# Performance work log

Measured on AMD Instinct MI355X. Metric: run time of the kernel, lower is better.

The kernel has to match this reference:

```python
import jax, jax.numpy as jnp
import numpy as np


def setup_inputs() -> dict:
    key = jax.random.key(0)
    ks = jax.random.split(key, 8)
    B, C, H, W = 4, 256, 56, 56
    Cq = C // 8
    s = 0.05  # small init scale for conv weights, like kaiming-ish for 1x1 convs
    return {
        "x": jax.random.normal(ks[0], (B, C, H, W), jnp.float32),
        "Wq": jax.random.normal(ks[1], (Cq, C), jnp.float32) * s,
        "bq": jax.random.normal(ks[2], (Cq,), jnp.float32) * s,
        "Wk": jax.random.normal(ks[3], (Cq, C), jnp.float32) * s,
        "bk": jax.random.normal(ks[4], (Cq,), jnp.float32) * s,
        "Wv": jax.random.normal(ks[5], (C, C), jnp.float32) * s,
        "bv": jax.random.normal(ks[6], (C,), jnp.float32) * s,
        "gamma": jax.random.normal(ks[7], (1,), jnp.float32),
    }


def reference(x, Wq, bq, Wk, bk, Wv, bv, gamma):
    B, C, H, W = x.shape
    N = H * W
    xf = x.reshape(B, C, N)  # flatten spatial

    # 1x1 convs == channel matmuls
    q = jnp.einsum('oc,bcn->bon', Wq, xf) + bq[None, :, None]   # [B,Cq,N]
    k = jnp.einsum('oc,bcn->bon', Wk, xf) + bk[None, :, None]   # [B,Cq,N]
    v = jnp.einsum('oc,bcn->bon', Wv, xf) + bv[None, :, None]   # [B,C,N]

    # lipschitz_norm from weights: u=||Q||_F, v=max row-norm of K^T, w=max row-norm of V^T
    u = jnp.linalg.norm(Wq)
    vn = jnp.max(jnp.linalg.norm(Wk.T, axis=1))
    wn = jnp.max(jnp.linalg.norm(Wv.T, axis=1))
    norm_value = jnp.maximum(u * vn, u * wn)  # maximum(u*v, v*u, u*w)

    # energy[b,i,j] = <q[:,i], k[:,j]>, scaled by custom Lipschitz norm
    energy = jnp.einsum('bci,bcj->bij', q, k) / norm_value      # [B,N,N]
    attention = jax.nn.softmax(energy, axis=-1)

    # out[b,c,i] = sum_j v[b,c,j] * attention[b,i,j]
    out = jnp.einsum('bcj,bij->bci', v, attention).reshape(B, C, H, W)

    # lipschitz_bound: exp(sqrt(3)) * sqrt(N/C) + 2*sqrt(6)
    bound = np.float32(np.exp(np.sqrt(3.0)) * np.sqrt(N / C) + 2.0 * np.sqrt(6.0))
    out = out / bound

    return gamma * out + x
```

## Files before the change

### kernel.cpp

```cpp
#include <hip/hip_runtime.h>

#define N_SP 3136
#define C_CH 256
#define CQ   32
#define NB   4
#define JT   64
#define NJT  49
#define QT   64
#define INV_BOUND 0.04051569f
#define LOG2E 1.44269504f

typedef __attribute__((ext_vector_type(8))) short bf16x8;
typedef __attribute__((ext_vector_type(4))) float f32x4;
typedef __attribute__((ext_vector_type(2))) long long l64x2;
typedef unsigned short u16;
typedef unsigned int   u32;
typedef unsigned char  u8;
typedef long long      l64;

#define MFMA16(a,b,c) __builtin_amdgcn_mfma_f32_16x16x32_bf16(a,b,c,0,0,0)
#define MFMA8(a,b,c)  __builtin_amdgcn_mfma_f32_16x16x32_bf8_fp8(a,b,c,0,0,0)

__device__ __forceinline__ u16 f2b(float f) {
    u32 u = __builtin_bit_cast(u32, f);
    u += 0x7fffu + ((u >> 16) & 1u);
    return (u16)(u >> 16);
}
__device__ __forceinline__ u8 f2fp8(float f) {
    return (u8)(__builtin_amdgcn_cvt_pk_fp8_f32(f, f, 0, false) & 0xff);
}
__device__ __forceinline__ void dma16(const void* g, void* l) {
    __builtin_amdgcn_global_load_lds((const __attribute__((address_space(1))) u32*)g,
                                     (__attribute__((address_space(3))) u32*)l, 16, 0, 0);
}
__device__ __forceinline__ void dma4(const void* g, void* l) {
    __builtin_amdgcn_global_load_lds((const __attribute__((address_space(1))) u32*)g,
                                     (__attribute__((address_space(3))) u32*)l, 4, 0, 0);
}

__global__ __launch_bounds__(256) void stage1_kernel(
    const float* __restrict__ x, const float* __restrict__ Wq,
    const float* __restrict__ Wk, const float* __restrict__ Wv,
    u8* __restrict__ xT, u8* __restrict__ Wqb, u8* __restrict__ Wkb,
    u8* __restrict__ Wvb, float* __restrict__ scale_out,
    float* __restrict__ kmax)
{
    __shared__ float smem[64 * 65];
    const int t = threadIdx.x;
    const int bid = blockIdx.x;

    if (bid < 784) {
        float (*tile)[65] = (float(*)[65])smem;
        const int xcd = bid & 7, slot = bid >> 3;
        const int b = xcd >> 1;
        const int i = slot * 2 + (xcd & 1);
        const int ct = i & 3, nt = i >> 2;
        const int c0 = ct * 64, n0 = nt * 64;
        const int cc = t >> 4, nn4 = (t & 15) * 4;
        #pragma unroll
        for (int k = 0; k < 4; ++k) {
            int cl = cc + k * 16;
            float4 v = *(const float4*)(x + (size_t)(b * C_CH + c0 + cl) * N_SP + n0 + nn4);
            tile[cl][nn4] = v.x; tile[cl][nn4 + 1] = v.y;
            tile[cl][nn4 + 2] = v.z; tile[cl][nn4 + 3] = v.w;
        }
        __syncthreads();
        const int c4 = (t & 15) * 4, nn = t >> 4;
        #pragma unroll
        for (int k = 0; k < 4; ++k) {
            int nl = nn + k * 16;
            ushort4 o;
            o.x = f2b(tile[c4 + 0][nl]); o.y = f2b(tile[c4 + 1][nl]);
            o.z = f2b(tile[c4 + 2][nl]); o.w = f2b(tile[c4 + 3][nl]);
            const int off = ((c0 + c4) * 2) ^ ((nl & 15) << 5);
            *(ushort4*)(xT + (size_t)(b * N_SP + n0 + nl) * 512 + off) = o;
        }
    } else if (bid < 864) {
        int idx = (bid - 784) * 256 + t;
        const float* src; u8* dst; int off;
        if (idx < 2048)      { src = Wq; dst = Wqb; off = idx; }
        else if (idx < 4096) { src = Wk; dst = Wkb; off = idx - 2048; }
        else                 { src = Wv; dst = Wvb; off = idx - 4096; }
        float4 v = *(const float4*)(src + off * 4);
        ushort4 o; o.x = f2b(v.x); o.y = f2b(v.y); o.z = f2b(v.z); o.w = f2b(v.w);
        const int row = off >> 6, inner = (off & 63) * 8;
        *(ushort4*)(dst + row * 512 + (inner ^ ((row & 15) << 5))) = o;
    } else {
        if (t < NB) kmax[t] = 0.f;
        float* red = smem;
        float u2 = 0.f;
        for (int i = t; i < CQ * C_CH; i += 256) { float w = Wq[i]; u2 += w * w; }
        red[t] = u2; __syncthreads();
        #pragma unroll
        for (int s = 128; s > 0; s >>= 1) { if (t < s) red[t] += red[t + s]; __syncthreads(); }
        float u2t = red[0]; __syncthreads();
        float vn2 = 0.f;
        for (int o = 0; o < CQ; ++o)   { float w = Wk[o * C_CH + t]; vn2 += w * w; }
        float wn2 = 0.f;
        for (int o = 0; o < C_CH; ++o) { float w = Wv[o * C_CH + t]; wn2 += w * w; }
        red[t] = fmaxf(vn2, wn2); __syncthreads();
        #pragma unroll
        for (int s = 128; s > 0; s >>= 1) { if (t < s) red[t] = fmaxf(red[t], red[t + s]); __syncthreads(); }
        if (t == 0) scale_out[0] = 1.0f / (sqrtf(u2t) * sqrtf(red[0]));
    }
}

__global__ __launch_bounds__(256) void qkv_mfma(
    const u8* __restrict__ xT, const u8* __restrict__ Wqb,
    const u8* __restrict__ Wkb, const u8* __restrict__ Wvb,
    const float* __restrict__ bq, const float* __restrict__ bk,
    const float* __restrict__ bv, const float* __restrict__ scale_p,
    u16* __restrict__ qT, u8* __restrict__ Kg, u8* __restrict__ Vg,
    float* __restrict__ qnorm, float* __restrict__ kmax)
{
    __shared__ __align__(16) u8 xTl[32768];
    __shared__ __align__(16) u8 Wl[32768];

    const int t = threadIdx.x;
    const int xcd = blockIdx.x & 7, slot = blockIdx.x >> 3;
    const int b = xcd >> 1;
    const int i = slot * 2 + (xcd & 1);
    if (i >= 245) return;
    const int split = i / 49, nt = i % 49;
    const int w = t >> 6, lane = t & 63, li = t & 15, g = (t >> 4) & 3;
    const int n = nt * 64 + w * 16 + li;
    const int r0 = (split - 1) * 64;
    const f32x4 zero = {0.f, 0.f, 0.f, 0.f};

    {
        const u8* xsrc = xT + (size_t)(b * N_SP + nt * 64) * 512;
        #pragma unroll
        for (int k = 0; k < 8; ++k)
            dma16(xsrc + w * 8192 + k * 1024 + lane * 16, xTl + w * 8192 + k * 1024);
        if (split == 0) {
            #pragma unroll
            for (int k = 0; k < 4; ++k)
                dma16(Wqb + w * 4096 + k * 1024 + lane * 16, Wl + w * 4096 + k * 1024);
            #pragma unroll
            for (int k = 0; k < 4; ++k)
                dma16(Wkb + w * 4096 + k * 1024 + lane * 16, Wl + 16384 + w * 4096 + k * 1024);
        } else {
            const u8* wsrc = Wvb + (size_t)r0 * 512;
            #pragma unroll
            for (int k = 0; k < 8; ++k)
                dma16(wsrc + w * 8192 + k * 1024 + lane * 16, Wl + w * 8192 + k * 1024);
        }
    }
    asm volatile("s_waitcnt vmcnt(0)" ::: "memory");
    __syncthreads();

    const int swz = li << 5;
    bf16x8 xf[8];
    #pragma unroll
    for (int ks = 0; ks < 8; ++ks)
        xf[ks] = *(const bf16x8*)(xTl + (w * 16 + li) * 512 + ((ks * 64 + 16 * g) ^ swz));

    if (split == 0) {
        f32x4 aq0 = zero, aq1 = zero, ak0 = zero, ak1 = zero;
        #pragma unroll
        for (int ks = 0; ks < 8; ++ks) {
            const int o = (ks * 64 + 16 * g) ^ swz;
            bf16x8 w0 = *(const bf16x8*)(Wl + li * 512 + o);
            bf16x8 w1 = *(const bf16x8*)(Wl + (16 + li) * 512 + o);
            bf16x8 w2 = *(const bf16x8*)(Wl + 16384 + li * 512 + o);
            bf16x8 w3 = *(const bf16x8*)(Wl + 16384 + (16 + li) * 512 + o);
            aq0 = MFMA16(w0, xf[ks], aq0);
            aq1 = MFMA16(w1, xf[ks], aq1);
            ak0 = MFMA16(w2, xf[ks], ak0);
            ak1 = MFMA16(w3, xf[ks], ak1);
        }
        const float scf = scale_p[0] * LOG2E;
        f32x4 bq0 = *(const f32x4*)(bq + 4 * g);
        f32x4 bq1 = *(const f32x4*)(bq + 16 + 4 * g);
        f32x4 bk0 = *(const f32x4*)(bk + 4 * g);
        f32x4 bk1 = *(const f32x4*)(bk + 16 + 4 * g);
        float qn2 = 0.f, kn2 = 0.f;
        ushort4 s0, s1;
        #pragma unroll
        for (int r = 0; r < 4; ++r) {
            float q0 = (aq0[r] + bq0[r]) * scf;
            float q1 = (aq1[r] + bq1[r]) * scf;
            qn2 += q0 * q0 + q1 * q1;
            ((u16*)&s0)[r] = f2b(q0); ((u16*)&s1)[r] = f2b(q1);
        }
        *(ushort4*)(qT + (size_t)(b * N_SP + n) * CQ + 4 * g)      = s0;
        *(ushort4*)(qT + (size_t)(b * N_SP + n) * CQ + 16 + 4 * g) = s1;
        #pragma unroll
        for (int r = 0; r < 4; ++r) {
            float k0 = ak0[r] + bk0[r];
            float k1 = ak1[r] + bk1[r];
            kn2 += k0 * k0 + k1 * k1;
            ((u16*)&s0)[r] = f2b(k0); ((u16*)&s1)[r] = f2b(k1);
        }
        u8* krow = Kg + ((size_t)b * N_SP + n) * 64;
        const int swn = ((n >> 1) & 3) << 4;
        *(ushort4*)(krow + ((8 * g) ^ swn))      = s0;
        *(ushort4*)(krow + ((32 + 8 * g) ^ swn)) = s1;

        qn2 += __shfl_xor(qn2, 16); qn2 += __shfl_xor(qn2, 32);
        kn2 += __shfl_xor(kn2, 16); kn2 += __shfl_xor(kn2, 32);
        if (g == 0) qnorm[b * N_SP + n] = sqrtf(qn2);
        float kn = sqrtf(kn2);
        #pragma unroll
        for (int d = 1; d < 16; d <<= 1) kn = fmaxf(kn, __shfl_xor(kn, d));
        if ((t & 63) == 0) atomicMax((int*)(kmax + b), __float_as_int(kn));
    } else {
        f32x4 a[4] = {zero, zero, zero, zero};
        #pragma unroll
        for (int ks = 0; ks < 8; ++ks) {
            const int o = (ks * 64 + 16 * g) ^ swz;
            #pragma unroll
            for (int fr = 0; fr < 4; ++fr) {
                bf16x8 wf = *(const bf16x8*)(Wl + (fr * 16 + li) * 512 + o);
                a[fr] = MFMA16(wf, xf[ks], a[fr]);
            }
        }
        const int jj = w * 16 + li;
        const int p = ((jj >> 5) & 1) * 8 + ((jj >> 3) & 3) * 16 + (jj & 7);
        u8* vtile = Vg + (size_t)(b * NJT + nt) * 16384;
        #pragma unroll
        for (int fr = 0; fr < 4; ++fr) {
            f32x4 bb = *(const f32x4*)(bv + r0 + fr * 16 + 4 * g);
            #pragma unroll
            for (int r = 0; r < 4; ++r) {
                const int c = r0 + fr * 16 + 4 * g + r;
                vtile[c * 64 + (p ^ (((c >> 1) & 3) << 4))] = f2fp8(a[fr][r] + bb[r]);
            }
        }
    }
}

__global__ __launch_bounds__(512) void attn_mfma(
    const u16* __restrict__ qT, const u8* __restrict__ Kg,
    const u8* __restrict__ Vg, const float* __restrict__ x,
    const float* __restrict__ gamma_p, const float* __restrict__ qnorm,
    const float* __restrict__ kmax, float* __restrict__ out)
{
    __shared__ __align__(16) u8 smem[86016];
    u8* const Vl = smem;
    u8* const Kl = smem + 65536;
    u8* const Pl = smem + 81920;

    const int t = threadIdx.x;
    const int w = t >> 6, li = t & 15, g = (t >> 4) & 3;
    const int jh = w & 3, qh = w >> 2;
    const int cw = w * 32;
    const int swz = ((li >> 1) & 3) << 4;

    const int xcd = blockIdx.x & 7, slot = blockIdx.x >> 3;
    const int b  = xcd >> 1;
    const int qt = slot * 2 + (xcd & 1);
    if (qt >= NJT) return;
    const int i0 = qt * QT;

    const u16* qTb = qT + (size_t)b * N_SP * CQ;
    const u8*  Kbb = Kg + (size_t)b * N_SP * 64;
    const u8*  Vbb = Vg + (size_t)b * NJT * 16384;
    const float kmb = kmax[b];
    const f32x4 zero = {0.f, 0.f, 0.f, 0.f};

    const int qA = 2 * qh, qB = 2 * qh + 1;
    const bf16x8 qfA = *(const bf16x8*)(qTb + (size_t)(i0 + qA * 16 + li) * CQ + 8 * g);
    const bf16x8 qfB = *(const bf16x8*)(qTb + (size_t)(i0 + qB * 16 + li) * CQ + 8 * g);
    const float mrA = qnorm[b * N_SP + i0 + qA * 16 + li] * kmb;
    const float mrB = qnorm[b * N_SP + i0 + qB * 16 + li] * kmb;

    f32x4 acc[4][2];
    #pragma unroll
    for (int qq = 0; qq < 4; ++qq) { acc[qq][0] = zero; acc[qq][1] = zero; }
    float lsA = 0.f, lsB = 0.f;

    #define ISSUE(jt_, s_) do {                                               \
        const u8* vsrc_ = Vbb + (size_t)(jt_) * 16384;                        \
        const u8* ksrc_ = Kbb + (size_t)(jt_) * 4096;                         \
        _Pragma("unroll")                                                     \
        for (int i_ = 0; i_ < 2; ++i_)                                        \
            dma16(vsrc_ + i_ * 8192 + t * 16,                                 \
                  Vl + (s_) * 16384 + i_ * 8192 + w * 1024);                  \
        _Pragma("unroll")                                                     \
        for (int i_ = 0; i_ < 2; ++i_)                                        \
            dma4(ksrc_ + i_ * 2048 + t * 4,                                   \
                 Kl + (s_) * 4096 + i_ * 2048 + w * 256);                     \
    } while (0)

    ISSUE(0, 0);
    ISSUE(1, 1);
    ISSUE(2, 2);

    const int p0 = ((jh >> 1) & 1) * 8 + ((jh * 2 + (g >> 1)) & 3) * 16 + 4 * (g & 1);

    for (int it = 0; it < NJT; ++it) {
        const int cur = it & 3;
        asm volatile("s_waitcnt vmcnt(8) lgkmcnt(0)" ::: "memory");
        __builtin_amdgcn_s_barrier();
        asm volatile("" ::: "memory");

        {
            int jn = it + 3; if (jn > NJT - 1) jn = NJT - 1;
            ISSUE(jn, (cur + 3) & 3);
        }

        const u8* Kc = Kl + cur * 4096;
        bf16x8 kf = *(const bf16x8*)(Kc + (jh * 16 + li) * 64 + ((16 * g) ^ swz));
        f32x4 sA = MFMA16(kf, qfA, zero);
        f32x4 sB = MFMA16(kf, qfB, zero);
        {
            float a0 = exp2f(sA[0] - mrA), a1 = exp2f(sA[1] - mrA);
            float a2 = exp2f(sA[2] - mrA), a3 = exp2f(sA[3] - mrA);
            lsA += (a0 + a1) + (a2 + a3);
            int pk = __builtin_amdgcn_cvt_pk_bf8_f32(a0, a1, 0, false);
            pk = __builtin_amdgcn_cvt_pk_bf8_f32(a2, a3, pk, true);
            *(u32*)(Pl + (qA * 16 + li) * 64 + (p0 ^ swz)) = (u32)pk;
            float b0 = exp2f(sB[0] - mrB), b1 = exp2f(sB[1] - mrB);
            float b2 = exp2f(sB[2] - mrB), b3 = exp2f(sB[3] - mrB);
            lsB += (b0 + b1) + (b2 + b3);
            pk = __builtin_amdgcn_cvt_pk_bf8_f32(b0, b1, 0, false);
            pk = __builtin_amdgcn_cvt_pk_bf8_f32(b2, b3, pk, true);
            *(u32*)(Pl + (qB * 16 + li) * 64 + (p0 ^ swz)) = (u32)pk;
        }
        asm volatile("s_waitcnt lgkmcnt(0)" ::: "memory");
        __builtin_amdgcn_s_barrier();
        asm volatile("" ::: "memory");

        const u8* Vc = Vl + cur * 16384;
        __builtin_amdgcn_s_setprio(1);
        l64x2 pa0 = *(const l64x2*)(Pl + (0 * 16 + li) * 64 + ((16 * g) ^ swz));
        l64x2 pa1 = *(const l64x2*)(Pl + (1 * 16 + li) * 64 + ((16 * g) ^ swz));
        l64x2 pa2 = *(const l64x2*)(Pl + (2 * 16 + li) * 64 + ((16 * g) ^ swz));
        l64x2 pa3 = *(const l64x2*)(Pl + (3 * 16 + li) * 64 + ((16 * g) ^ swz));
        l64x2 v0  = *(const l64x2*)(Vc + (cw + li) * 64 + ((16 * g) ^ swz));
        l64x2 v1  = *(const l64x2*)(Vc + (cw + 16 + li) * 64 + ((16 * g) ^ swz));
        acc[0][0] = MFMA8(pa0[0], v0[0], acc[0][0]);
        acc[0][1] = MFMA8(pa0[0], v1[0], acc[0][1]);
        acc[1][0] = MFMA8(pa1[0], v0[0], acc[1][0]);
        acc[1][1] = MFMA8(pa1[0], v1[0], acc[1][1]);
        acc[2][0] = MFMA8(pa2[0], v0[0], acc[2][0]);
        acc[2][1] = MFMA8(pa2[0], v1[0], acc[2][1]);
        acc[3][0] = MFMA8(pa3[0], v0[0], acc[3][0]);
        acc[3][1] = MFMA8(pa3[0], v1[0], acc[3][1]);
        acc[0][0] = MFMA8(pa0[1], v0[1], acc[0][0]);
        acc[0][1] = MFMA8(pa0[1], v1[1], acc[0][1]);
        acc[1][0] = MFMA8(pa1[1], v0[1], acc[1][0]);
        acc[1][1] = MFMA8(pa1[1], v1[1], acc[1][1]);
        acc[2][0] = MFMA8(pa2[1], v0[1], acc[2][0]);
        acc[2][1] = MFMA8(pa2[1], v1[1], acc[2][1]);
        acc[3][0] = MFMA8(pa3[1], v0[1], acc[3][0]);
        acc[3][1] = MFMA8(pa3[1], v1[1], acc[3][1]);
        __builtin_amdgcn_s_setprio(0);
    }
    #undef ISSUE

    lsA += __shfl_xor(lsA, 16); lsA += __shfl_xor(lsA, 32);
    lsB += __shfl_xor(lsB, 16); lsB += __shfl_xor(lsB, 32);
    __syncthreads();
    float* red       = (float*)Pl;
    float* red_final = (float*)(Pl + 1024);
    if ((t & 63) < 16) {
        red[w * 32 + li]      = lsA;
        red[w * 32 + 16 + li] = lsB;
    }
    __syncthreads();
    if (t < 64) {
        const int h = t >> 4, l2 = t & 15;
        float s = 0.f;
        #pragma unroll
        for (int jw = 0; jw < 4; ++jw)
            s += red[((h >> 1) * 4 + jw) * 32 + (h & 1) * 16 + l2];
        red_final[t] = s;
    }
    __syncthreads();

    const float gsc = gamma_p[0] * INV_BOUND;
    #pragma unroll
    for (int qq = 0; qq < 4; ++qq) {
        f32x4 lsv = *(const f32x4*)(red_final + qq * 16 + 4 * g);
        f32x4 rinv;
        #pragma unroll
        for (int r = 0; r < 4; ++r) rinv[r] = gsc / lsv[r];
        #pragma unroll
        for (int cf = 0; cf < 2; ++cf) {
            const int c = cw + cf * 16 + li;
            const size_t base = ((size_t)b * C_CH + c) * N_SP + i0 + qq * 16 + 4 * g;
            float4 xv = *(const float4*)(x + base);
            float4 o;
            o.x = acc[qq][cf][0] * rinv[0] + xv.x;
            o.y = acc[qq][cf][1] * rinv[1] + xv.y;
            o.z = acc[qq][cf][2] * rinv[2] + xv.z;
            o.w = acc[qq][cf][3] * rinv[3] + xv.w;
            *(float4*)(out + base) = o;
        }
    }
}

extern "C" void kernel_launch(void* const* d_in, const int* in_sizes, int n_in,
                              void* d_out, int out_size, void* d_ws, size_t ws_size,
                              hipStream_t stream)
{
    const float* x  = (const float*)d_in[0];
    const float* Wq = (const float*)d_in[1];
    const float* bq = (const float*)d_in[2];
    const float* Wk = (const float*)d_in[3];
    const float* bk = (const float*)d_in[4];
    const float* Wv = (const float*)d_in[5];
    const float* bv = (const float*)d_in[6];
    const float* gm = (const float*)d_in[7];
    float* out = (float*)d_out;
    float* ws  = (float*)d_ws;

    float* scale = ws;
    float* kmax  = ws + 4;
    float* qnorm = ws + 8;
    u8* Wqb = (u8*)(ws + 8 + NB * N_SP);
    u8* Wkb = Wqb + 32 * 512;
    u8* Wvb = Wkb + 32 * 512;
    u8* xT  = Wvb + 256 * 512;
    u16* qT = (u16*)(xT + (size_t)NB * N_SP * 512);
    u8* Kg  = (u8*)(qT + (size_t)NB * N_SP * CQ);
    u8* Vg  = Kg + (size_t)NB * N_SP * 64;

    stage1_kernel<<<865, 256, 0, stream>>>(x, Wq, Wk, Wv, xT, Wqb, Wkb, Wvb, scale, kmax);
    qkv_mfma<<<984, 256, 0, stream>>>(xT, Wqb, Wkb, Wvb, bq, bk, bv, scale, qT, Kg, Vg, qnorm, kmax);
    attn_mfma<<<200, 512, 0, stream>>>(qT, Kg, Vg, x, gm, qnorm, kmax, out);
}
```

Measured before the change: 87.97 us.

## Split attention channels across two blocks to double grid parallelism

Result: slower. 93.10 us (+5.8%).

```diff
diff --git a/kernel.cpp b/kernel.cpp
--- a/kernel.cpp
+++ b/kernel.cpp
@@ -32,10 +32,6 @@
 __device__ __forceinline__ void dma16(const void* g, void* l) {
     __builtin_amdgcn_global_load_lds((const __attribute__((address_space(1))) u32*)g,
                                      (__attribute__((address_space(3))) u32*)l, 16, 0, 0);
-}
-__device__ __forceinline__ void dma4(const void* g, void* l) {
-    __builtin_amdgcn_global_load_lds((const __attribute__((address_space(1))) u32*)g,
-                                     (__attribute__((address_space(3))) u32*)l, 4, 0, 0);
 }
 
 __global__ __launch_bounds__(256) void stage1_kernel(
@@ -230,32 +226,30 @@
     }
 }
 
-__global__ __launch_bounds__(512) void attn_mfma(
+__global__ __launch_bounds__(512, 6) void attn_mfma(
     const u16* __restrict__ qT, const u8* __restrict__ Kg,
     const u8* __restrict__ Vg, const float* __restrict__ x,
     const float* __restrict__ gamma_p, const float* __restrict__ qnorm,
     const float* __restrict__ kmax, float* __restrict__ out)
 {
-    __shared__ __align__(16) u8 smem[86016];
+    __shared__ __align__(16) u8 smem[40960];
     u8* const Vl = smem;
-    u8* const Kl = smem + 65536;
-    u8* const Pl = smem + 81920;
+    u8* const Kl = smem + 24576;
+    u8* const Pl = smem + 36864;
 
     const int t = threadIdx.x;
     const int w = t >> 6, li = t & 15, g = (t >> 4) & 3;
     const int jh = w & 3, qh = w >> 2;
-    const int cw = w * 32;
     const int swz = ((li >> 1) & 3) << 4;
 
-    const int xcd = blockIdx.x & 7, slot = blockIdx.x >> 3;
-    const int b  = xcd >> 1;
-    const int qt = slot * 2 + (xcd & 1);
-    if (qt >= NJT) return;
+    const int bid = blockIdx.x;
+    const int b = bid / 98, rem = bid % 98;
+    const int qt = rem >> 1, h = rem & 1;
     const int i0 = qt * QT;
 
     const u16* qTb = qT + (size_t)b * N_SP * CQ;
     const u8*  Kbb = Kg + (size_t)b * N_SP * 64;
-    const u8*  Vbb = Vg + (size_t)b * NJT * 16384;
+    const u8*  Vbb = Vg + (size_t)b * NJT * 16384 + h * 8192;
     const float kmb = kmax[b];
     const f32x4 zero = {0.f, 0.f, 0.f, 0.f};
 
@@ -265,39 +259,35 @@
     const float mrA = qnorm[b * N_SP + i0 + qA * 16 + li] * kmb;
     const float mrB = qnorm[b * N_SP + i0 + qB * 16 + li] * kmb;
 
-    f32x4 acc[4][2];
+    f32x4 acc[4];
     #pragma unroll
-    for (int qq = 0; qq < 4; ++qq) { acc[qq][0] = zero; acc[qq][1] = zero; }
+    for (int qq = 0; qq < 4; ++qq) acc[qq] = zero;
     float lsA = 0.f, lsB = 0.f;
 
     #define ISSUE(jt_, s_) do {                                               \
-        const u8* vsrc_ = Vbb + (size_t)(jt_) * 16384;                        \
-        const u8* ksrc_ = Kbb + (size_t)(jt_) * 4096;                         \
-        _Pragma("unroll")                                                     \
-        for (int i_ = 0; i_ < 2; ++i_)                                        \
-            dma16(vsrc_ + i_ * 8192 + t * 16,                                 \
-                  Vl + (s_) * 16384 + i_ * 8192 + w * 1024);                  \
-        _Pragma("unroll")                                                     \
-        for (int i_ = 0; i_ < 2; ++i_)                                        \
-            dma4(ksrc_ + i_ * 2048 + t * 4,                                   \
-                 Kl + (s_) * 4096 + i_ * 2048 + w * 256);                     \
+        dma16(Vbb + (size_t)(jt_) * 16384 + t * 16,                           \
+              Vl + (s_) * 8192 + w * 1024);                                   \
+        if (t < 256)                                                          \
+            dma16(Kbb + (size_t)(jt_) * 4096 + t * 16,                        \
+                  Kl + (s_) * 4096 + w * 1024);                               \
     } while (0)
 
     ISSUE(0, 0);
     ISSUE(1, 1);
-    ISSUE(2, 2);
 
     const int p0 = ((jh >> 1) & 1) * 8 + ((jh * 2 + (g >> 1)) & 3) * 16 + 4 * (g & 1);
 
+    int cur = 0;
     for (int it = 0; it < NJT; ++it) {
-        const int cur = it & 3;
-        asm volatile("s_waitcnt vmcnt(8) lgkmcnt(0)" ::: "memory");
+        if (w < 4) asm volatile("s_waitcnt vmcnt(2) lgkmcnt(0)" ::: "memory");
+        else       asm volatile("s_waitcnt vmcnt(1) lgkmcnt(0)" ::: "memory");
         __builtin_amdgcn_s_barrier();
         asm volatile("" ::: "memory");
 
         {
-            int jn = it + 3; if (jn > NJT - 1) jn = NJT - 1;
-            ISSUE(jn, (cur + 3) & 3);
+            int jn = it + 2; if (jn > NJT - 1) jn = NJT - 1;
+            int s2 = cur + 2; if (s2 >= 3) s2 -= 3;
+            ISSUE(jn, s2);
         }
 
         const u8* Kc = Kl + cur * 4096;
@@ -322,31 +312,24 @@
         __builtin_amdgcn_s_barrier();
         asm volatile("" ::: "memory");
 
-        const u8* Vc = Vl + cur * 16384;
+        const u8* Vc = Vl + cur * 8192;
         __builtin_amdgcn_s_setprio(1);
         l64x2 pa0 = *(const l64x2*)(Pl + (0 * 16 + li) * 64 + ((16 * g) ^ swz));
         l64x2 pa1 = *(const l64x2*)(Pl + (1 * 16 + li) * 64 + ((16 * g) ^ swz));
         l64x2 pa2 = *(const l64x2*)(Pl + (2 * 16 + li) * 64 + ((16 * g) ^ swz));
         l64x2 pa3 = *(const l64x2*)(Pl + (3 * 16 + li) * 64 + ((16 * g) ^ swz));
-        l64x2 v0  = *(const l64x2*)(Vc + (cw + li) * 64 + ((16 * g) ^ swz));
-        l64x2 v1  = *(const l64x2*)(Vc + (cw + 16 + li) * 64 + ((16 * g) ^ swz));
-        acc[0][0] = MFMA8(pa0[0], v0[0], acc[0][0]);
-        acc[0][1] = MFMA8(pa0[0], v1[0], acc[0][1]);
-        acc[1][0] = MFMA8(pa1[0], v0[0], acc[1][0]);
-        acc[1][1] = MFMA8(pa1[0], v1[0], acc[1][1]);
-        acc[2][0] = MFMA8(pa2[0], v0[0], acc[2][0]);
-        acc[2][1] = MFMA8(pa2[0], v1[0], acc[2][1]);
-        acc[3][0] = MFMA8(pa3[0], v0[0], acc[3][0]);
-        acc[3][1] = MFMA8(pa3[0], v1[0], acc[3][1]);
-        acc[0][0] = MFMA8(pa0[1], v0[1], acc[0][0]);
-        acc[0][1] = MFMA8(pa0[1], v1[1], acc[0][1]);
-        acc[1][0] = MFMA8(pa1[1], v0[1], acc[1][0]);
-        acc[1][1] = MFMA8(pa1[1], v1[1], acc[1][1]);
-        acc[2][0] = MFMA8(pa2[1], v0[1], acc[2][0]);
-        acc[2][1] = MFMA8(pa2[1], v1[1], acc[2][1]);
-        acc[3][0] = MFMA8(pa3[1], v0[1], acc[3][0]);
-        acc[3][1] = MFMA8(pa3[1], v1[1], acc[3][1]);
+        l64x2 v0  = *(const l64x2*)(Vc + (w * 16 + li) * 64 + ((16 * g) ^ swz));
+        acc[0] = MFMA8(pa0[0], v0[0], acc[0]);
+        acc[1] = MFMA8(pa1[0], v0[0], acc[1]);
+        acc[2] = MFMA8(pa2[0], v0[0], acc[2]);
+        acc[3] = MFMA8(pa3[0], v0[0], acc[3]);
+        acc[0] = MFMA8(pa0[1], v0[1], acc[0]);
+        acc[1] = MFMA8(pa1[1], v0[1], acc[1]);
+        acc[2] = MFMA8(pa2[1], v0[1], acc[2]);
+        acc[3] = MFMA8(pa3[1], v0[1], acc[3]);
         __builtin_amdgcn_s_setprio(0);
+
+        ++cur; if (cur == 3) cur = 0;
     }
     #undef ISSUE
 
@@ -361,34 +344,31 @@
     }
     __syncthreads();
     if (t < 64) {
-        const int h = t >> 4, l2 = t & 15;
+        const int hh = t >> 4, l2 = t & 15;
         float s = 0.f;
         #pragma unroll
         for (int jw = 0; jw < 4; ++jw)
-            s += red[((h >> 1) * 4 + jw) * 32 + (h & 1) * 16 + l2];
+            s += red[((hh >> 1) * 4 + jw) * 32 + (hh & 1) * 16 + l2];
         red_final[t] = s;
     }
     __syncthreads();
 
     const float gsc = gamma_p[0] * INV_BOUND;
+    const int c = h * 128 + w * 16 + li;
     #pragma unroll
     for (int qq = 0; qq < 4; ++qq) {
         f32x4 lsv = *(const f32x4*)(red_final + qq * 16 + 4 * g);
         f32x4 rinv;
         #pragma unroll
         for (int r = 0; r < 4; ++r) rinv[r] = gsc / lsv[r];
-        #pragma unroll
-        for (int cf = 0; cf < 2; ++cf) {
-            const int c = cw + cf * 16 + li;
-            const size_t base = ((size_t)b * C_CH + c) * N_SP + i0 + qq * 16 + 4 * g;
-            float4 xv = *(const float4*)(x + base);
-            float4 o;
-            o.x = acc[qq][cf][0] * rinv[0] + xv.x;
-            o.y = acc[qq][cf][1] * rinv[1] + xv.y;
-            o.z = acc[qq][cf][2] * rinv[2] + xv.z;
-            o.w = acc[qq][cf][3] * rinv[3] + xv.w;
-            *(float4*)(out + base) = o;
-        }
+        const size_t base = ((size_t)b * C_CH + c) * N_SP + i0 + qq * 16 + 4 * g;
+        float4 xv = *(const float4*)(x + base);
+        float4 o;
+        o.x = acc[qq][0] * rinv[0] + xv.x;
+        o.y = acc[qq][1] * rinv[1] + xv.y;
+        o.z = acc[qq][2] * rinv[2] + xv.z;
+        o.w = acc[qq][3] * rinv[3] + xv.w;
+        *(float4*)(out + base) = o;
     }
 }
 
@@ -420,5 +400,5 @@
 
     stage1_kernel<<<865, 256, 0, stream>>>(x, Wq, Wk, Wv, xT, Wqb, Wkb, Wvb, scale, kmax);
     qkv_mfma<<<984, 256, 0, stream>>>(xT, Wqb, Wkb, Wvb, bq, bk, bv, scale, qT, Kg, Vg, qnorm, kmax);
-    attn_mfma<<<200, 512, 0, stream>>>(qT, Kg, Vg, x, gm, qnorm, kmax, out);
-}
+    attn_mfma<<<392, 512, 0, stream>>>(qT, Kg, Vg, x, gm, qnorm, kmax, out);
+}
```
